# Performance work log

Hardware: AMD Instinct MI355X
Metric: run time of the kernel (lower is better)

## Reference

```python
import jax, jax.numpy as jnp
import numpy as np

B, T, D, H, C = 64, 512, 128, 512, 256  # batch, seq_len, input_dim, rnn_dim, clf hidden


def _lstm_cell(x, h, c, Wih, Whh, b):
    # PyTorch gate order: i, f, g, o; b = bias_ih + bias_hh
    gates = x @ Wih.T + h @ Whh.T + b  # [B, 4H]
    i, f, g, o = jnp.split(gates, 4, axis=-1)
    c = jax.nn.sigmoid(f) * c + jax.nn.sigmoid(i) * jnp.tanh(g)
    h = jax.nn.sigmoid(o) * jnp.tanh(c)
    return h, c


def _run_lstm2(xs, state, p0, p1):
    # xs: [B, T, in]; state: (h0, c0, h1, c1) each [B, H]
    def step(carry, x_t):
        h0, c0, h1, c1 = carry
        h0, c0 = _lstm_cell(x_t, h0, c0, *p0)
        h1, c1 = _lstm_cell(h0, h1, c1, *p1)
        return (h0, c0, h1, c1), h1
    state, ys = jax.lax.scan(step, state, jnp.swapaxes(xs, 0, 1))
    return jnp.swapaxes(ys, 0, 1), state


def setup_inputs() -> dict:
    key = jax.random.key(0)
    ks = jax.random.split(key, 18)
    s = 0.04  # ~1/sqrt(H), matches torch LSTM init scale
    w = lambda k, shape: (jax.random.normal(k, shape, jnp.float32) * s)
    inp = {
        "x": jax.random.uniform(ks[0], (B, T, D), dtype=jnp.float32),
        "y": (jax.random.uniform(ks[1], (B, T, D), dtype=jnp.float32) > 0.9).astype(jnp.float32),
        "enc_Wih0": w(ks[2], (4 * H, D)), "enc_Whh0": w(ks[3], (4 * H, H)), "enc_b0": w(ks[4], (4 * H,)),
        "enc_Wih1": w(ks[5], (4 * H, H)), "enc_Whh1": w(ks[6], (4 * H, H)), "enc_b1": w(ks[7], (4 * H,)),
        "dec_Wih0": w(ks[8], (4 * H, D)), "dec_Whh0": w(ks[9], (4 * H, H)), "dec_b0": w(ks[10], (4 * H,)),
        "dec_Wih1": w(ks[11], (4 * H, H)), "dec_Whh1": w(ks[12], (4 * H, H)), "dec_b1": w(ks[13], (4 * H,)),
        "clf_W1": w(ks[14], (C, H)), "clf_b1": w(ks[15], (C,)),
        "clf_W2": w(ks[16], (D, C)), "clf_b2": w(ks[17], (D,)),
    }
    return inp


def reference(x, y, enc_Wih0, enc_Whh0, enc_b0, enc_Wih1, enc_Whh1, enc_b1,
              dec_Wih0, dec_Whh0, dec_b0, dec_Wih1, dec_Whh1, dec_b1,
              clf_W1, clf_b1, clf_W2, clf_b2):
    Bc = x.shape[0]
    z = jnp.zeros((Bc, H), x.dtype)
    # encoder: only final (h, c) of both layers is used
    _, state = _run_lstm2(x, (z, z, z, z),
                          (enc_Wih0, enc_Whh0, enc_b0), (enc_Wih1, enc_Whh1, enc_b1))
    # decoder under full teacher forcing: steps t=1..T-1 consume y[:, t-1]
    dec_out, _ = _run_lstm2(y[:, :-1], state,
                            (dec_Wih0, dec_Whh0, dec_b0), (dec_Wih1, dec_Whh1, dec_b1))
    hid = jax.nn.relu(dec_out @ clf_W1.T + clf_b1)          # [B, T-1, C]
    logits = hid @ clf_W2.T + clf_b2                        # [B, T-1, D]
    # outputs[:, 0] stays zero, as in the torch loop starting at t=1
    return jnp.concatenate([jnp.zeros_like(logits[:, :1]), logits], axis=1)
```

## Files before the change

kernel.cpp:

```cpp
#include <hip/hip_runtime.h>
#include <hip/hip_bf16.h>
#include <stdint.h>

#define SMEM_BYTES 150528

using short8  = __attribute__((ext_vector_type(8))) short;
using f32x4   = __attribute__((ext_vector_type(4))) float;
using u32x4   = __attribute__((ext_vector_type(4))) unsigned int;

#define OXBF 0u
#define OYBF 8388608u
#define OWE0 16777216u
#define OWD0 (OWE0 + 2621440u)
#define OWE1 (OWD0 + 2621440u)
#define OWD1 (OWE1 + 4194304u)
#define OWC1 (OWD1 + 4194304u)
#define OWC2 (OWC1 + 262144u)
#define OA0  (OWC2 + 65536u)
#define OB0  (OA0 + 2097152u)
#define OA1  (OB0 + 2097152u)
#define OB1  (OA1 + 2097152u)
#define OHP  (OB1 + 2097152u)
#define OFLG (OHP + 1048576u)
#define OFC1 (OFLG + 4096u)
#define OFH  (OFLG + 8192u)
#define OFL  (OFLG + 9216u)
#define OPRB (OFLG + 16384u)
#define OVOT (OFLG + 32768u)

#define GUARD (1<<19)

static __device__ __forceinline__ unsigned short f2bf(float f){
  union { float f; unsigned u; } v; v.f = f;
  unsigned r = v.u + 0x7FFFu + ((v.u >> 16) & 1u);
  return (unsigned short)(r >> 16);
}
static __device__ __forceinline__ float sigm(float x){ return 1.f/(1.f+__expf(-x)); }
static __device__ __forceinline__ float tanh_(float x){ return 1.f - 2.f/(__expf(2.f*x)+1.f); }

static __device__ __forceinline__ u32x4 ld_r16(const void* p, bool loc){
  u32x4 v;
  if (loc) asm volatile("global_load_dwordx4 %0, %1, off sc0"     : "=v"(v) : "v"(p) : "memory");
  else     asm volatile("global_load_dwordx4 %0, %1, off sc0 sc1" : "=v"(v) : "v"(p) : "memory");
  return v;
}
static __device__ __forceinline__ void st_r16(void* p, u32x4 v, bool loc){
  if (loc) asm volatile("global_store_dwordx4 %0, %1, off sc0"     :: "v"(p), "v"(v) : "memory");
  else     asm volatile("global_store_dwordx4 %0, %1, off sc0 sc1" :: "v"(p), "v"(v) : "memory");
}
static __device__ __forceinline__ unsigned ld_f4(const void* p, bool loc){
  unsigned v;
  if (loc) asm volatile("global_load_dword %0, %1, off sc0\n\ts_waitcnt vmcnt(0)"     : "=v"(v) : "v"(p) : "memory");
  else     asm volatile("global_load_dword %0, %1, off sc0 sc1\n\ts_waitcnt vmcnt(0)" : "=v"(v) : "v"(p) : "memory");
  return v;
}
static __device__ __forceinline__ void st_f4(void* p, unsigned v, bool loc){
  if (loc) asm volatile("global_store_dword %0, %1, off sc0"     :: "v"(p), "v"(v) : "memory");
  else     asm volatile("global_store_dword %0, %1, off sc0 sc1" :: "v"(p), "v"(v) : "memory");
}
static __device__ __forceinline__ unsigned ld_cg4(const void* p){ return ld_f4(p, false); }
static __device__ __forceinline__ void st_cg4(void* p, unsigned v){ st_f4(p, v, false); }
static __device__ __forceinline__ void drain_vm(){
  asm volatile("s_waitcnt vmcnt(0)" ::: "memory");
}
static __device__ __forceinline__ bool isS(u32x4 v){
  return (v[0]==0xFFFFFFFFu) | (v[1]==0xFFFFFFFFu) | (v[2]==0xFFFFFFFFu) | (v[3]==0xFFFFFFFFu);
}

__global__ void k_init(float* __restrict__ out, uint8_t* __restrict__ ws){
  int i = blockIdx.x*blockDim.x + threadIdx.x;
  int ns = gridDim.x*blockDim.x;
  uint32_t* r = (uint32_t*)(ws + OA0);
  const int nring = (4*2097152 + 1048576)/4;
  for (int k=i; k<nring; k+=ns) r[k] = 0xFFFFFFFFu;
  uint32_t* fl = (uint32_t*)(ws + OFLG);
  for (int k=i; k<49152/4; k+=ns) fl[k] = 0u;
  for (int k=i; k<64*128; k+=ns) out[(size_t)(k>>7)*(512*128) + (k&127)] = 0.f;
}

__global__ void k_cvt(const float* __restrict__ x, const float* __restrict__ y,
                      uint8_t* __restrict__ ws){
  unsigned short* xb = (unsigned short*)(ws + OXBF);
  unsigned short* yb = (unsigned short*)(ws + OYBF);
  const int n = 64*512*128;
  int i = blockIdx.x*blockDim.x + threadIdx.x, ns = gridDim.x*blockDim.x;
  for (int k=i; k<n; k+=ns){ xb[k] = f2bf(x[k]); yb[k] = f2bf(y[k]); }
}

__global__ void k_swzgate(const float* __restrict__ Wih, const float* __restrict__ Whh,
                          uint8_t* __restrict__ ws, size_t dstOff, int Kin, int KC, int NKK, int mode){
  unsigned short* dst = (unsigned short*)(ws + dstOff);
  const int total = 2048 * (KC*4);
  int i = blockIdx.x*blockDim.x + threadIdx.x, ns = gridDim.x*blockDim.x;
  for (int idx=i; idx<total; idx+=ns){
    int j = idx & 7;
    int lane = (idx >> 3) & 63;
    int t = idx >> 9;
    int g = t & 3; t >>= 2;
    int kk = t % NKK; t /= NKK;
    int w = t & 3; int ub = t >> 2;
    int off = ((lane>>4)<<3) + j;
    int k = mode ? (kk==0 ? w*32 + off : 128 + w*128 + (kk-1)*32 + off)
                 : (w*KC + kk*32 + off);
    int u = ub*16 + (lane&15);
    int row = g*512 + u;
    float v = (k < Kin) ? Wih[(size_t)row*Kin + k] : Whh[(size_t)row*512 + (k-Kin)];
    dst[idx] = f2bf(v);
  }
}

__global__ void k_swzclf(const float* __restrict__ W, uint8_t* __restrict__ ws,
                         size_t dstOff, int nwgs, int Kw, int Ktot){
  unsigned short* dst = (unsigned short*)(ws + dstOff);
  const int NKK = Kw/32;
  const int total = nwgs*4*NKK*64*8;
  int i = blockIdx.x*blockDim.x + threadIdx.x, ns = gridDim.x*blockDim.x;
  for (int idx=i; idx<total; idx+=ns){
    int j = idx & 7;
    int lane = (idx >> 3) & 63;
    int t = idx >> 9;
    int kk = t % NKK; t /= NKK;
    int w = t & 3; int wg = t >> 2;
    int k = w*Kw + kk*32 + ((lane>>4)<<3) + j;
    int col = wg*16 + (lane&15);
    dst[idx] = f2bf(W[(size_t)col*Ktot + k]);
  }
}

__launch_bounds__(256, 1)
__global__ void k_seq(uint8_t* __restrict__ ws,
                      const float* __restrict__ eb0, const float* __restrict__ eb1,
                      const float* __restrict__ db0, const float* __restrict__ db1,
                      const float* __restrict__ cb1, const float* __restrict__ cb2,
                      float* __restrict__ out){
  __shared__ uint8_t smem[SMEM_BYTES];
  const int wg = blockIdx.x, tid = threadIdx.x;
  const int w = tid>>6, l = tid&63, lr = l&15, lg = l>>4;
  const int xcd = wg & 7, j = wg >> 3;

  int role;
  if (xcd < 2) role = 0;
  else if (xcd < 4) role = 1;
  else if (xcd == 4 && j < 16) role = 2;
  else if (xcd == 4 && j < 24) role = 3;
  else return;

  const unsigned short* xb = (const unsigned short*)(ws+OXBF);
  const unsigned short* yb = (const unsigned short*)(ws+OYBF);
  unsigned short* A0e = (unsigned short*)(ws+OA0);
  unsigned short* B0e = (unsigned short*)(ws+OB0);
  unsigned short* A1e = (unsigned short*)(ws+OA1);
  unsigned short* B1e = (unsigned short*)(ws+OB1);
  unsigned short* hpr = (unsigned short*)(ws+OHP);

  short8* BL = (short8*)smem;
  float*  P0 = (float*)(smem + 131072);
  float*  P1 = (float*)(smem + 139776);
  unsigned short* HS = (unsigned short*)(smem + 148480);

  const u32x4 S4 = (u32x4){0xFFFFFFFFu,0xFFFFFFFFu,0xFFFFFFFFu,0xFFFFFFFFu};
  const u32x4 Z4 = (u32x4){0u,0u,0u,0u};

  bool loc;
  {
    const int n   = (role <= 1) ? 32 : 24;
    const int bas = (role <= 1) ? xcd : 4;
    if (w == 0){
      bool ok = true;
      #pragma unroll 1
      for (int gen = 1; gen <= 3; ++gen){
        if (l == 0) st_f4(ws + OPRB + (size_t)wg*64u, (unsigned)gen, true);
        if (l < n){
          const void* p = ws + OPRB + (size_t)(bas + 8*l)*64u;
          int spins = 0; unsigned e;
          do { e = ld_f4(p, true); } while ((int)e < gen && ++spins < 1024);
          if ((int)e < gen) ok = false;
        }
      }
      unsigned long long b1 = __ballot(ok);
      bool wgok = (b1 == ~0ULL);
      if (l == 0) st_f4(ws + OVOT + (size_t)wg*64u, wgok ? 2u : 1u, false);
      bool vok = wgok;
      if (l < n){
        const void* p = ws + OVOT + (size_t)(bas + 8*l)*64u;
        unsigned v;
        do { v = ld_f4(p, false); } while (v == 0u);
        vok = vok && (v == 2u);
      }
      unsigned long long b2 = __ballot(vok);
      if (l == 0) *(int*)HS = (b2 == ~0ULL) ? 1 : 0;
    }
    __syncthreads();
    loc = (*(volatile int*)HS) != 0;
    __syncthreads();
  }

  auto loadB = [&](size_t srcOff, int bytes){
    const u32x4* s = (const u32x4*)(ws + srcOff);
    u32x4* d = (u32x4*)smem;
    for (int i = tid; i < bytes/16; i += 256) d[i] = s[i];
  };

  if (role <= 1){
    const bool isC0 = (role == 0);
    const int bt = isC0 ? xcd : xcd-2, ub = j;
    const int u = tid&15, ug = ub*16 + u;
    const int bbytes = isC0 ? 81920 : 131072;
    unsigned short* OWN0 = loc ? A0e : B0e;

    float be[4], bd[4];
    {
      const float* e = isC0 ? eb0 : eb1;
      const float* d = isC0 ? db0 : db1;
      #pragma unroll
      for (int g=0; g<4; ++g){ be[g] = e[g*512+ug]; bd[g] = d[g*512+ug]; }
    }
    loadB((isC0 ? (size_t)OWE0 : (size_t)OWE1) + (size_t)ub*bbytes, bbytes);
    float cS0 = 0.f, cS1 = 0.f;
    __syncthreads();

    for (int t = 0; t < 1023; ++t){
      if (t == 512){
        __syncthreads();
        loadB((isC0 ? (size_t)OWD0 : (size_t)OWD1) + (size_t)ub*bbytes, bbytes);
        __syncthreads();
      }

      const int slotW = t&31, slotR = (t+31)&31;

      f32x4 acc[2][4];
      #pragma unroll
      for (int m=0;m<2;++m)
        #pragma unroll
        for (int g=0;g<4;++g) acc[m][g] = (f32x4){0.f,0.f,0.f,0.f};

      if (isC0){
        const unsigned short* xs = (t<512) ? xb : yb;
        const int tt = (t<512) ? t : t-512;
        short8 ax[2];
        #pragma unroll
        for (int m=0;m<2;++m){
          const int b = bt*32 + m*16 + lr;
          ax[m] = *(const short8*)(xs + ((size_t)b*512 + tt)*128 + w*32 + (lg<<3));
        }
        u32x4 ah[4][2];
        if (t > 0){
          const unsigned short* base = OWN0 + (size_t)slotR*64*512;
          int gd = 0; bool bad;
          do {
            #pragma unroll
            for (int kk=0; kk<4; ++kk)
              #pragma unroll
              for (int m=0;m<2;++m){
                const int b = bt*32 + m*16 + lr;
                ah[kk][m] = ld_r16(base + (size_t)b*512 + w*128 + kk*32 + (lg<<3), loc);
              }
            drain_vm();
            __builtin_amdgcn_sched_barrier(0);
            bad = false;
            #pragma unroll
            for (int kk=0; kk<4; ++kk)
              #pragma unroll
              for (int m=0;m<2;++m) bad |= isS(ah[kk][m]);
            if (bad) __builtin_amdgcn_s_sleep(1);
          } while (bad && ++gd < GUARD);
          __builtin_amdgcn_sched_barrier(0);
        } else {
          #pragma unroll
          for (int kk=0; kk<4; ++kk)
            #pragma unroll
            for (int m=0;m<2;++m) ah[kk][m] = Z4;
        }
        #pragma unroll
        for (int g=0;g<4;++g){
          short8 bf = BL[((w*5+0)*4+g)*64 + l];
          acc[0][g] = __builtin_amdgcn_mfma_f32_16x16x32_bf16(ax[0], bf, acc[0][g],0,0,0);
          acc[1][g] = __builtin_amdgcn_mfma_f32_16x16x32_bf16(ax[1], bf, acc[1][g],0,0,0);
        }
        #pragma unroll
        for (int kk=1; kk<5; ++kk)
          #pragma unroll
          for (int g=0;g<4;++g){
            short8 bf = BL[((w*5+kk)*4+g)*64 + l];
            acc[0][g] = __builtin_amdgcn_mfma_f32_16x16x32_bf16(__builtin_bit_cast(short8, ah[kk-1][0]), bf, acc[0][g],0,0,0);
            acc[1][g] = __builtin_amdgcn_mfma_f32_16x16x32_bf16(__builtin_bit_cast(short8, ah[kk-1][1]), bf, acc[1][g],0,0,0);
          }
      } else {
        u32x4 a[8][2];
        const bool wv01 = (w < 2);
        if (wv01 || t > 0){
          const unsigned short* base;
          bool myloc;
          if (wv01){ base = B0e + (size_t)slotW*64*512; myloc = false; }
          else {
            base = (loc ? A1e : (((t-1) >= 512) ? B1e : A1e)) + (size_t)slotR*64*512;
            myloc = loc;
          }
          const int kbase = wv01 ? (w*256) : (w*256 - 512);
          int gd = 0; bool bad;
          do {
            #pragma unroll
            for (int kk=0; kk<8; ++kk)
              #pragma unroll
              for (int m=0;m<2;++m){
                const int b = bt*32 + m*16 + lr;
                a[kk][m] = ld_r16(base + (size_t)b*512 + kbase + kk*32 + (lg<<3), myloc);
              }
            drain_vm();
            __builtin_amdgcn_sched_barrier(0);
            bad = false;
            #pragma unroll
            for (int kk=0; kk<8; ++kk)
              #pragma unroll
              for (int m=0;m<2;++m) bad |= isS(a[kk][m]);
            if (bad) __builtin_amdgcn_s_sleep(1);
          } while (bad && ++gd < GUARD);
          __builtin_amdgcn_sched_barrier(0);
        } else {
          #pragma unroll
          for (int kk=0; kk<8; ++kk)
            #pragma unroll
            for (int m=0;m<2;++m) a[kk][m] = Z4;
        }
        #pragma unroll
        for (int kk=0; kk<8; ++kk)
          #pragma unroll
          for (int g=0;g<4;++g){
            short8 bf = BL[((w*8+kk)*4+g)*64 + l];
            acc[0][g] = __builtin_amdgcn_mfma_f32_16x16x32_bf16(__builtin_bit_cast(short8, a[kk][0]), bf, acc[0][g],0,0,0);
            acc[1][g] = __builtin_amdgcn_mfma_f32_16x16x32_bf16(__builtin_bit_cast(short8, a[kk][1]), bf, acc[1][g],0,0,0);
          }
      }

      {
        float* P = (w&1) ? P1 : P0;
        if (w < 2){
          #pragma unroll
          for (int m=0;m<2;++m)
            #pragma unroll
            for (int g=0;g<4;++g)
              #pragma unroll
              for (int r=0;r<4;++r)
                P[(m*16 + (lg<<2) + r)*68 + g*16 + lr] = acc[m][g][r];
        }
        __syncthreads();
        if (w >= 2){
          #pragma unroll
          for (int m=0;m<2;++m)
            #pragma unroll
            for (int g=0;g<4;++g)
              #pragma unroll
              for (int r=0;r<4;++r)
                P[(m*16 + (lg<<2) + r)*68 + g*16 + lr] += acc[m][g][r];
        }
        __syncthreads();
      }

      if (w == 0 && (t & 7) == 0){
        drain_vm();
        __builtin_amdgcn_sched_barrier(0);
        if (isC0){
          if (t >= 24 && l < 32){
            const void* p = ws + OFC1 + (size_t)(bt*32+l)*64;
            const int need = (t-22 < 1) ? 1 : t-22;
            int v, gd = 0;
            do { v = (int)ld_f4(p, false); if (v < need) __builtin_amdgcn_s_sleep(2); }
            while (v < need && ++gd < GUARD);
          }
        } else {
          if (t >= 536 && l < 16){
            const void* p = ws + OFH + (size_t)l*64;
            const int need = (t-534 < 1) ? 1 : t-534;
            int v, gd = 0;
            do { v = (int)ld_f4(p, false); if (v < need) __builtin_amdgcn_s_sleep(2); }
            while (v < need && ++gd < GUARD);
          }
        }
        if (t >= 8){
          const int row = l>>1, half = l&1;
          #pragma unroll
          for (int a=2; a<=9; ++a){
            const int cs = (t+a)&31;
            const size_t off = ((size_t)cs*64 + bt*32 + row)*512 + ub*16 + half*8;
            if (isC0){
              st_r16(OWN0 + off, S4, loc);
              if (loc) st_r16(B0e + off, S4, false);
            } else {
              st_r16(loc ? A1e + off : (((t+a-32) >= 512) ? B1e + off : A1e + off), S4, loc ? true : false);
              if (loc && (t+a) >= 544) st_r16(B1e + off, S4, false);
            }
          }
        }
      }

      const float* bias = (t<512) ? be : bd;
      #pragma unroll
      for (int s=0;s<2;++s){
        const int row = (tid>>4) + s*16;
        const int pi = row*68 + u;
        float gi = P0[pi]      + P1[pi]      + bias[0];
        float gf = P0[pi+16]   + P1[pi+16]   + bias[1];
        float gg = P0[pi+32]   + P1[pi+32]   + bias[2];
        float go = P0[pi+48]   + P1[pi+48]   + bias[3];
        float cprev = s ? cS1 : cS0;
        float c = sigm(gf)*cprev + sigm(gi)*tanh_(gg);
        if (s) cS1 = c; else cS0 = c;
        float h = sigm(go)*tanh_(c);
        HS[row*16 + u] = f2bf(h);
      }
      __syncthreads();
      if (tid < 64){
        u32x4 v = *(const u32x4*)(HS + tid*8);
        const int row = tid>>1, half = tid&1;
        const size_t off = ((size_t)slotW*64 + bt*32 + row)*512 + ub*16 + half*8;
        if (isC0){
          st_r16(OWN0 + off, v, loc);
          if (loc) st_r16(B0e + off, v, false);
        } else {
          if (loc){
            st_r16(A1e + off, v, true);
            if (t >= 512) st_r16(B1e + off, v, false);
          } else {
            st_r16(((t >= 512) ? B1e : A1e) + off, v, false);
          }
        }
      }
      if (!isC0 && tid == 0)
        st_f4(ws + OFC1 + (size_t)(bt*32+ub)*64, (unsigned)(t+1), false);
    }
  } else if (role == 2){
    const int hwg = j;
    const int u = tid&15, col = hwg*16 + u;
    const float bc = cb1[col];
    loadB((size_t)OWC1 + (size_t)hwg*16384, 16384);
    __syncthreads();
    for (int t2 = 0; t2 < 511; ++t2){
      const int slot = (512+t2)&31;

      u32x4 a[4][4];
      const unsigned short* base = B1e + (size_t)slot*64*512;
      int gd = 0; bool bad;
      do {
        #pragma unroll
        for (int kk=0; kk<4; ++kk)
          #pragma unroll
          for (int m=0;m<4;++m)
            a[kk][m] = ld_r16(base + (size_t)(m*16+lr)*512 + w*128 + kk*32 + (lg<<3), false);
        drain_vm();
        __builtin_amdgcn_sched_barrier(0);
        bad = false;
        #pragma unroll
        for (int kk=0; kk<4; ++kk)
          #pragma unroll
          for (int m=0;m<4;++m) bad |= isS(a[kk][m]);
        if (bad) __builtin_amdgcn_s_sleep(1);
      } while (bad && ++gd < GUARD);
      __builtin_amdgcn_sched_barrier(0);
      f32x4 ha[4];
      #pragma unroll
      for (int m=0;m<4;++m) ha[m] = (f32x4){0.f,0.f,0.f,0.f};
      #pragma unroll
      for (int kk=0; kk<4; ++kk){
        short8 bf = BL[(w*4+kk)*64 + l];
        #pragma unroll
        for (int m=0;m<4;++m)
          ha[m] = __builtin_amdgcn_mfma_f32_16x16x32_bf16(__builtin_bit_cast(short8, a[kk][m]), bf, ha[m],0,0,0);
      }
      {
        float* P = (w&1) ? P1 : P0;
        if (w < 2){
          #pragma unroll
          for (int m=0;m<4;++m)
            #pragma unroll
            for (int r=0;r<4;++r)
              P[(m*16 + (lg<<2) + r)*20 + lr] = ha[m][r];
        }
        __syncthreads();
        if (w >= 2){
          #pragma unroll
          for (int m=0;m<4;++m)
            #pragma unroll
            for (int r=0;r<4;++r)
              P[(m*16 + (lg<<2) + r)*20 + lr] += ha[m][r];
        }
        __syncthreads();
      }
      if (w == 0 && (t2 & 7) == 0){
        drain_vm();
        __builtin_amdgcn_sched_barrier(0);
        if (t2 >= 24 && l < 8){
          const void* p = ws + OFL + (size_t)l*64;
          const int need = (t2-22 < 1) ? 1 : t2-22;
          int v, g2 = 0;
          do { v = (int)ld_f4(p, loc); if (v < need) __builtin_amdgcn_s_sleep(2); }
          while (v < need && ++g2 < GUARD);
        }
        if (t2 >= 8){
          #pragma unroll
          for (int a=2; a<=9; ++a){
            const int cs = (t2+a)&31;
            #pragma unroll
            for (int q=0;q<2;++q)
              st_r16(hpr + ((size_t)cs*64 + l)*256 + hwg*16 + q*8, S4, loc);
          }
        }
      }
      #pragma unroll
      for (int s=0;s<4;++s){
        const int row = (tid>>4) + s*16;
        float v = P0[row*20+u] + P1[row*20+u] + bc;
        HS[row*16 + u] = f2bf(fmaxf(v, 0.f));
      }
      __syncthreads();
      if (tid < 128){
        u32x4 v = *(const u32x4*)(HS + tid*8);
        const int row = tid>>1, half = tid&1;
        st_r16(hpr + ((size_t)(t2&31)*64 + row)*256 + hwg*16 + half*8, v, loc);
      }
      if (tid == 0) st_f4(ws + OFH + (size_t)hwg*64, (unsigned)(t2+1), false);
    }
  } else {
    const int lwg = j - 16;
    const int u = tid&15, col = lwg*16 + u;
    const float bc = cb2[col];
    loadB((size_t)OWC2 + (size_t)lwg*8192, 8192);
    __syncthreads();
    for (int t3 = 0; t3 < 511; ++t3){
      const int slot = t3&31;
      u32x4 a[2][4];
      const unsigned short* base = hpr + (size_t)slot*64*256;
      int gd = 0; bool bad;
      do {
        #pragma unroll
        for (int kk=0; kk<2; ++kk)
          #pragma unroll
          for (int m=0;m<4;++m)
            a[kk][m] = ld_r16(base + (size_t)(m*16+lr)*256 + w*64 + kk*32 + (lg<<3), loc);
        drain_vm();
        __builtin_amdgcn_sched_barrier(0);
        bad = false;
        #pragma unroll
        for (int kk=0; kk<2; ++kk)
          #pragma unroll
          for (int m=0;m<4;++m) bad |= isS(a[kk][m]);
        if (bad) __builtin_amdgcn_s_sleep(1);
      } while (bad && ++gd < GUARD);
      __builtin_amdgcn_sched_barrier(0);
      f32x4 la[4];
      #pragma unroll
      for (int m=0;m<4;++m) la[m] = (f32x4){0.f,0.f,0.f,0.f};
      #pragma unroll
      for (int kk=0; kk<2; ++kk){
        short8 bf = BL[(w*2+kk)*64 + l];
        #pragma unroll
        for (int m=0;m<4;++m)
          la[m] = __builtin_amdgcn_mfma_f32_16x16x32_bf16(__builtin_bit_cast(short8, a[kk][m]), bf, la[m],0,0,0);
      }
      {
        float* P = (w&1) ? P1 : P0;
        if (w < 2){
          #pragma unroll
          for (int m=0;m<4;++m)
            #pragma unroll
            for (int r=0;r<4;++r)
              P[(m*16 + (lg<<2) + r)*20 + lr] = la[m][r];
        }
        __syncthreads();
        if (w >= 2){
          #pragma unroll
          for (int m=0;m<4;++m)
            #pragma unroll
            for (int r=0;r<4;++r)
              P[(m*16 + (lg<<2) + r)*20 + lr] += la[m][r];
        }
        __syncthreads();
      }
      #pragma unroll
      for (int s=0;s<4;++s){
        const int row = (tid>>4) + s*16;
        float v = P0[row*20+u] + P1[row*20+u] + bc;
        out[((size_t)row*512 + (t3+1))*128 + col] = v;
      }
      if (tid == 0) st_f4(ws + OFL + (size_t)lwg*64, (unsigned)(t3+1), loc);
    }
  }
}

extern "C" void kernel_launch(void* const* d_in, const int* in_sizes, int n_in,
                              void* d_out, int out_size, void* d_ws, size_t ws_size,
                              hipStream_t stream){
  const float* x   = (const float*)d_in[0];
  const float* y   = (const float*)d_in[1];
  const float* eW0 = (const float*)d_in[2];
  const float* eU0 = (const float*)d_in[3];
  const float* eb0 = (const float*)d_in[4];
  const float* eW1 = (const float*)d_in[5];
  const float* eU1 = (const float*)d_in[6];
  const float* eb1 = (const float*)d_in[7];
  const float* dW0 = (const float*)d_in[8];
  const float* dU0 = (const float*)d_in[9];
  const float* db0 = (const float*)d_in[10];
  const float* dW1 = (const float*)d_in[11];
  const float* dU1 = (const float*)d_in[12];
  const float* db1 = (const float*)d_in[13];
  const float* cW1 = (const float*)d_in[14];
  const float* cb1 = (const float*)d_in[15];
  const float* cW2 = (const float*)d_in[16];
  const float* cb2 = (const float*)d_in[17];
  float* out = (float*)d_out;
  uint8_t* ws = (uint8_t*)d_ws;
  (void)in_sizes; (void)n_in; (void)out_size; (void)ws_size;

  k_init<<<dim3(256), dim3(256), 0, stream>>>(out, ws);
  k_cvt<<<dim3(2048), dim3(256), 0, stream>>>(x, y, ws);
  k_swzgate<<<dim3(1280), dim3(256), 0, stream>>>(eW0, eU0, ws, (size_t)OWE0, 128, 160, 5, 1);
  k_swzgate<<<dim3(1280), dim3(256), 0, stream>>>(dW0, dU0, ws, (size_t)OWD0, 128, 160, 5, 1);
  k_swzgate<<<dim3(2048), dim3(256), 0, stream>>>(eW1, eU1, ws, (size_t)OWE1, 512, 256, 8, 0);
  k_swzgate<<<dim3(2048), dim3(256), 0, stream>>>(dW1, dU1, ws, (size_t)OWD1, 512, 256, 8, 0);
  k_swzclf<<<dim3(256), dim3(256), 0, stream>>>(cW1, ws, (size_t)OWC1, 16, 128, 512);
  k_swzclf<<<dim3(64),  dim3(256), 0, stream>>>(cW2, ws, (size_t)OWC2, 8, 64, 256);
  k_seq<<<dim3(256), dim3(256), 0, stream>>>(ws, eb0, eb1, db0, db1, cb1, cb2, out);
}
```

Before: 5.209 ms.

## Replace sentinel-poisoned ring polling with per-slot counter flags

The old scheme marked ring slots with an all-ones sentinel, re-stored that sentinel ahead of use, and polled the full data tiles until no sentinel remained. The new scheme keeps a small array of per-slot, per-producer counters. Producers drain their stores and then write the step number. Consumers spin on one dword per lane with a ballot, and only read the data tiles once every counter is ready. This removes the sentinel init and re-poison stores and the wide retry loads, at the cost of an extra drain, a barrier, and a second round trip (flag, then data) on each step.

```diff
diff --git a/kernel.cpp b/kernel.cpp
--- a/kernel.cpp
+++ b/kernel.cpp
@@ -27,6 +27,11 @@
 #define OFL  (OFLG + 9216u)
 #define OPRB (OFLG + 16384u)
 #define OVOT (OFLG + 32768u)
+#define OCA0 (OFLG + 49152u)
+#define OCB0 (OCA0 + 131072u)
+#define OCA1 (OCB0 + 131072u)
+#define OCB1 (OCA1 + 131072u)
+#define OCHP (OCB1 + 131072u)
 
 #define GUARD (1<<19)
 
@@ -58,23 +63,16 @@
   if (loc) asm volatile("global_store_dword %0, %1, off sc0"     :: "v"(p), "v"(v) : "memory");
   else     asm volatile("global_store_dword %0, %1, off sc0 sc1" :: "v"(p), "v"(v) : "memory");
 }
-static __device__ __forceinline__ unsigned ld_cg4(const void* p){ return ld_f4(p, false); }
-static __device__ __forceinline__ void st_cg4(void* p, unsigned v){ st_f4(p, v, false); }
 static __device__ __forceinline__ void drain_vm(){
   asm volatile("s_waitcnt vmcnt(0)" ::: "memory");
-}
-static __device__ __forceinline__ bool isS(u32x4 v){
-  return (v[0]==0xFFFFFFFFu) | (v[1]==0xFFFFFFFFu) | (v[2]==0xFFFFFFFFu) | (v[3]==0xFFFFFFFFu);
 }
 
 __global__ void k_init(float* __restrict__ out, uint8_t* __restrict__ ws){
   int i = blockIdx.x*blockDim.x + threadIdx.x;
   int ns = gridDim.x*blockDim.x;
-  uint32_t* r = (uint32_t*)(ws + OA0);
-  const int nring = (4*2097152 + 1048576)/4;
-  for (int k=i; k<nring; k+=ns) r[k] = 0xFFFFFFFFu;
   uint32_t* fl = (uint32_t*)(ws + OFLG);
-  for (int k=i; k<49152/4; k+=ns) fl[k] = 0u;
+  const int nfl = (49152 + 5*131072)/4;
+  for (int k=i; k<nfl; k+=ns) fl[k] = 0u;
   for (int k=i; k<64*128; k+=ns) out[(size_t)(k>>7)*(512*128) + (k&127)] = 0.f;
 }
 
@@ -158,7 +156,6 @@
   float*  P1 = (float*)(smem + 139776);
   unsigned short* HS = (unsigned short*)(smem + 148480);
 
-  const u32x4 S4 = (u32x4){0xFFFFFFFFu,0xFFFFFFFFu,0xFFFFFFFFu,0xFFFFFFFFu};
   const u32x4 Z4 = (u32x4){0u,0u,0u,0u};
 
   bool loc;
@@ -207,6 +204,7 @@
     const int u = tid&15, ug = ub*16 + u;
     const int bbytes = isC0 ? 81920 : 131072;
     unsigned short* OWN0 = loc ? A0e : B0e;
+    const uint32_t OWNC0 = loc ? OCA0 : OCB0;
 
     float be[4], bd[4];
     {
@@ -225,7 +223,6 @@
         loadB((isC0 ? (size_t)OWD0 : (size_t)OWD1) + (size_t)ub*bbytes, bbytes);
         __syncthreads();
       }
-
       const int slotW = t&31, slotR = (t+31)&31;
 
       f32x4 acc[2][4];
@@ -245,25 +242,23 @@
         }
         u32x4 ah[4][2];
         if (t > 0){
-          const unsigned short* base = OWN0 + (size_t)slotR*64*512;
+          const void* cp = ws + OWNC0 + ((size_t)slotR*64 + bt*32 + w*8 + (l&7))*64u;
           int gd = 0; bool bad;
           do {
-            #pragma unroll
-            for (int kk=0; kk<4; ++kk)
-              #pragma unroll
-              for (int m=0;m<2;++m){
-                const int b = bt*32 + m*16 + lr;
-                ah[kk][m] = ld_r16(base + (size_t)b*512 + w*128 + kk*32 + (lg<<3), loc);
-              }
-            drain_vm();
-            __builtin_amdgcn_sched_barrier(0);
-            bad = false;
-            #pragma unroll
-            for (int kk=0; kk<4; ++kk)
-              #pragma unroll
-              for (int m=0;m<2;++m) bad |= isS(ah[kk][m]);
+            unsigned cv = ld_f4(cp, loc);
+            bad = (__ballot((l < 8) && ((int)cv < t)) != 0ULL);
             if (bad) __builtin_amdgcn_s_sleep(1);
           } while (bad && ++gd < GUARD);
+          __builtin_amdgcn_sched_barrier(0);
+          const unsigned short* base = OWN0 + (size_t)slotR*64*512;
+          #pragma unroll
+          for (int kk=0; kk<4; ++kk)
+            #pragma unroll
+            for (int m=0;m<2;++m){
+              const int b = bt*32 + m*16 + lr;
+              ah[kk][m] = ld_r16(base + (size_t)b*512 + w*128 + kk*32 + (lg<<3), loc);
+            }
+          drain_vm();
           __builtin_amdgcn_sched_barrier(0);
         } else {
           #pragma unroll
@@ -289,32 +284,33 @@
         u32x4 a[8][2];
         const bool wv01 = (w < 2);
         if (wv01 || t > 0){
-          const unsigned short* base;
-          bool myloc;
-          if (wv01){ base = B0e + (size_t)slotW*64*512; myloc = false; }
+          const unsigned short* base; uint32_t canb; bool myloc; int tgt; int slot_;
+          if (wv01){ base = B0e; canb = OCB0; myloc = false; tgt = t+1; slot_ = slotW; }
           else {
-            base = (loc ? A1e : (((t-1) >= 512) ? B1e : A1e)) + (size_t)slotR*64*512;
-            myloc = loc;
+            const bool enc = ((t-1) < 512);
+            base  = loc ? A1e : (enc ? A1e : B1e);
+            canb  = loc ? OCA1 : (enc ? OCA1 : OCB1);
+            myloc = loc; tgt = t; slot_ = slotR;
           }
-          const int kbase = wv01 ? (w*256) : (w*256 - 512);
+          const int qb = wv01 ? (16*w) : (16*(w-2));
+          const void* cp = ws + canb + ((size_t)slot_*64 + bt*32 + qb + (l&15))*64u;
           int gd = 0; bool bad;
           do {
-            #pragma unroll
-            for (int kk=0; kk<8; ++kk)
-              #pragma unroll
-              for (int m=0;m<2;++m){
-                const int b = bt*32 + m*16 + lr;
-                a[kk][m] = ld_r16(base + (size_t)b*512 + kbase + kk*32 + (lg<<3), myloc);
-              }
-            drain_vm();
-            __builtin_amdgcn_sched_barrier(0);
-            bad = false;
-            #pragma unroll
-            for (int kk=0; kk<8; ++kk)
-              #pragma unroll
-              for (int m=0;m<2;++m) bad |= isS(a[kk][m]);
+            unsigned cv = ld_f4(cp, myloc);
+            bad = (__ballot((l < 16) && ((int)cv < tgt)) != 0ULL);
             if (bad) __builtin_amdgcn_s_sleep(1);
           } while (bad && ++gd < GUARD);
+          __builtin_amdgcn_sched_barrier(0);
+          const unsigned short* pb = base + (size_t)slot_*64*512;
+          const int kbase = wv01 ? (w*256) : (w*256 - 512);
+          #pragma unroll
+          for (int kk=0; kk<8; ++kk)
+            #pragma unroll
+            for (int m=0;m<2;++m){
+              const int b = bt*32 + m*16 + lr;
+              a[kk][m] = ld_r16(pb + (size_t)b*512 + kbase + kk*32 + (lg<<3), myloc);
+            }
+          drain_vm();
           __builtin_amdgcn_sched_barrier(0);
         } else {
           #pragma unroll
@@ -376,21 +372,6 @@
             while (v < need && ++gd < GUARD);
           }
         }
-        if (t >= 8){
-          const int row = l>>1, half = l&1;
-          #pragma unroll
-          for (int a=2; a<=9; ++a){
-            const int cs = (t+a)&31;
-            const size_t off = ((size_t)cs*64 + bt*32 + row)*512 + ub*16 + half*8;
-            if (isC0){
-              st_r16(OWN0 + off, S4, loc);
-              if (loc) st_r16(B0e + off, S4, false);
-            } else {
-              st_r16(loc ? A1e + off : (((t+a-32) >= 512) ? B1e + off : A1e + off), S4, loc ? true : false);
-              if (loc && (t+a) >= 544) st_r16(B1e + off, S4, false);
-            }
-          }
-        }
       }
 
       const float* bias = (t<512) ? be : bd;
@@ -424,6 +405,21 @@
             st_r16(((t >= 512) ? B1e : A1e) + off, v, false);
           }
         }
+        drain_vm();
+        if (tid == 0){
+          const size_t coff = ((size_t)slotW*64 + bt*32 + ub)*64u;
+          if (isC0){
+            if (loc) st_f4(ws + OCA0 + coff, (unsigned)(t+1), true);
+            st_f4(ws + OCB0 + coff, (unsigned)(t+1), false);
+          } else {
+            if (loc){
+              st_f4(ws + OCA1 + coff, (unsigned)(t+1), true);
+              if (t >= 512) st_f4(ws + OCB1 + coff, (unsigned)(t+1), false);
+            } else {
+              st_f4(ws + ((t >= 512) ? OCB1 : OCA1) + coff, (unsigned)(t+1), false);
+            }
+          }
+        }
       }
       if (!isC0 && tid == 0)
         st_f4(ws + OFC1 + (size_t)(bt*32+ub)*64, (unsigned)(t+1), false);
@@ -436,25 +432,25 @@
     __syncthreads();
     for (int t2 = 0; t2 < 511; ++t2){
       const int slot = (512+t2)&31;
-
+      const int tgt = 513 + t2;
+      {
+        const void* cp = ws + OCB1 + ((size_t)slot*64 + ((l>>3)&1)*32 + 8*w + (l&7))*64u;
+        int gd = 0; bool bad;
+        do {
+          unsigned cv = ld_f4(cp, false);
+          bad = (__ballot((l < 16) && ((int)cv < tgt)) != 0ULL);
+          if (bad) __builtin_amdgcn_s_sleep(1);
+        } while (bad && ++gd < GUARD);
+        __builtin_amdgcn_sched_barrier(0);
+      }
       u32x4 a[4][4];
       const unsigned short* base = B1e + (size_t)slot*64*512;
-      int gd = 0; bool bad;
-      do {
-        #pragma unroll
-        for (int kk=0; kk<4; ++kk)
-          #pragma unroll
-          for (int m=0;m<4;++m)
-            a[kk][m] = ld_r16(base + (size_t)(m*16+lr)*512 + w*128 + kk*32 + (lg<<3), false);
-        drain_vm();
-        __builtin_amdgcn_sched_barrier(0);
-        bad = false;
-        #pragma unroll
-        for (int kk=0; kk<4; ++kk)
-          #pragma unroll
-          for (int m=0;m<4;++m) bad |= isS(a[kk][m]);
-        if (bad) __builtin_amdgcn_s_sleep(1);
-      } while (bad && ++gd < GUARD);
+      #pragma unroll
+      for (int kk=0; kk<4; ++kk)
+        #pragma unroll
+        for (int m=0;m<4;++m)
+          a[kk][m] = ld_r16(base + (size_t)(m*16+lr)*512 + w*128 + kk*32 + (lg<<3), false);
+      drain_vm();
       __builtin_amdgcn_sched_barrier(0);
       f32x4 ha[4];
       #pragma unroll
@@ -495,15 +491,6 @@
           do { v = (int)ld_f4(p, loc); if (v < need) __builtin_amdgcn_s_sleep(2); }
           while (v < need && ++g2 < GUARD);
         }
-        if (t2 >= 8){
-          #pragma unroll
-          for (int a=2; a<=9; ++a){
-            const int cs = (t2+a)&31;
-            #pragma unroll
-            for (int q=0;q<2;++q)
-              st_r16(hpr + ((size_t)cs*64 + l)*256 + hwg*16 + q*8, S4, loc);
-          }
-        }
       }
       #pragma unroll
       for (int s=0;s<4;++s){
@@ -517,7 +504,12 @@
         const int row = tid>>1, half = tid&1;
         st_r16(hpr + ((size_t)(t2&31)*64 + row)*256 + hwg*16 + half*8, v, loc);
       }
-      if (tid == 0) st_f4(ws + OFH + (size_t)hwg*64, (unsigned)(t2+1), false);
+      drain_vm();
+      __syncthreads();
+      if (tid == 0){
+        st_f4(ws + OCHP + ((size_t)(t2&31)*64 + hwg)*64u, (unsigned)(t2+1), loc);
+        st_f4(ws + OFH + (size_t)hwg*64, (unsigned)(t2+1), false);
+      }
     }
   } else {
     const int lwg = j - 16;
@@ -527,24 +519,25 @@
     __syncthreads();
     for (int t3 = 0; t3 < 511; ++t3){
       const int slot = t3&31;
+      const int tgt = t3+1;
+      {
+        const void* cp = ws + OCHP + ((size_t)slot*64 + 4*w + (l&3))*64u;
+        int gd = 0; bool bad;
+        do {
+          unsigned cv = ld_f4(cp, loc);
+          bad = (__ballot((l < 4) && ((int)cv < tgt)) != 0ULL);
+          if (bad) __builtin_amdgcn_s_sleep(1);
+        } while (bad && ++gd < GUARD);
+        __builtin_amdgcn_sched_barrier(0);
+      }
       u32x4 a[2][4];
       const unsigned short* base = hpr + (size_t)slot*64*256;
-      int gd = 0; bool bad;
-      do {
-        #pragma unroll
-        for (int kk=0; kk<2; ++kk)
-          #pragma unroll
-          for (int m=0;m<4;++m)
-            a[kk][m] = ld_r16(base + (size_t)(m*16+lr)*256 + w*64 + kk*32 + (lg<<3), loc);
-        drain_vm();
-        __builtin_amdgcn_sched_barrier(0);
-        bad = false;
-        #pragma unroll
-        for (int kk=0; kk<2; ++kk)
-          #pragma unroll
-          for (int m=0;m<4;++m) bad |= isS(a[kk][m]);
-        if (bad) __builtin_amdgcn_s_sleep(1);
-      } while (bad && ++gd < GUARD);
+      #pragma unroll
+      for (int kk=0; kk<2; ++kk)
+        #pragma unroll
+        for (int m=0;m<4;++m)
+          a[kk][m] = ld_r16(base + (size_t)(m*16+lr)*256 + w*64 + kk*32 + (lg<<3), loc);
+      drain_vm();
       __builtin_amdgcn_sched_barrier(0);
       f32x4 la[4];
       #pragma unroll
```

Result: slower. 5.323 ms (+2.2%).
